# Kernel tuning notes

Measured on AMD Instinct MI355X. Metric: run time of the kernel, lower is better.

## Reference

```python
import jax, jax.numpy as jnp
import numpy as np

D_MODEL, N_HEADS, D_FF = 512, 8, 2048
B, L = 2, 2048


def layer_norm(x, g, b, eps=1e-5):
    mu = jnp.mean(x, axis=-1, keepdims=True)
    var = jnp.mean(jnp.square(x - mu), axis=-1, keepdims=True)
    return (x - mu) * jax.lax.rsqrt(var + eps) * g + b


def setup_inputs() -> dict:
    key = jax.random.key(0)
    ks = jax.random.split(key, 16)
    s = 1.0 / np.sqrt(D_MODEL)
    sf = 1.0 / np.sqrt(D_FF)
    return {
        "x": jax.random.normal(ks[0], (B, L, D_MODEL), jnp.float32),
        "Wq": jax.random.normal(ks[1], (D_MODEL, D_MODEL), jnp.float32) * s,
        "bq": jnp.zeros((D_MODEL,), jnp.float32),
        "Wk": jax.random.normal(ks[2], (D_MODEL, D_MODEL), jnp.float32) * s,
        "bk": jnp.zeros((D_MODEL,), jnp.float32),
        "Wv": jax.random.normal(ks[3], (D_MODEL, D_MODEL), jnp.float32) * s,
        "bv": jnp.zeros((D_MODEL,), jnp.float32),
        "Wo": jax.random.normal(ks[4], (D_MODEL, D_MODEL), jnp.float32) * s,
        "bo": jnp.zeros((D_MODEL,), jnp.float32),
        "W1": jax.random.normal(ks[5], (D_FF, D_MODEL), jnp.float32) * s,   # conv1 k=1 -> linear
        "b1": jnp.zeros((D_FF,), jnp.float32),
        "W2": jax.random.normal(ks[6], (D_MODEL, D_FF), jnp.float32) * sf,  # conv2 k=1 -> linear
        "b2": jnp.zeros((D_MODEL,), jnp.float32),
        "g1": jnp.ones((D_MODEL,), jnp.float32),
        "be1": jnp.zeros((D_MODEL,), jnp.float32),
        "g2": jnp.ones((D_MODEL,), jnp.float32),
        "be2": jnp.zeros((D_MODEL,), jnp.float32),
    }


def reference(x, Wq, bq, Wk, bk, Wv, bv, Wo, bo, W1, b1, W2, b2, g1, be1, g2, be2):
    Bx, Lx, D = x.shape
    H = N_HEADS
    dk = D // H
    # projections -> [B, L, H, dk]
    q = (x @ Wq.T + bq).reshape(Bx, Lx, H, dk)
    k = (x @ Wk.T + bk).reshape(Bx, Lx, H, dk)
    v = (x @ Wv.T + bv).reshape(Bx, Lx, H, dk)
    scale = 1.0 / jnp.sqrt(jnp.asarray(dk, x.dtype))
    scores = jnp.einsum('blhd,bshd->bhls', q, k)  # full LxL score tensor (as in source)
    A = jax.nn.softmax(scale * scores, axis=-1)
    out = jnp.einsum('bhls,bshd->blhd', A, v).reshape(Bx, Lx, D)
    attn_out = out @ Wo.T + bo
    # residual + norm1 (dropout is identity in eval)
    x1 = layer_norm(x + attn_out, g1, be1)
    # FFN: conv1d with kernel_size=1 == pointwise linear
    y = jax.nn.relu(x1 @ W1.T + b1)
    y = y @ W2.T + b2
    return layer_norm(x1 + y, g2, be2)
```

## Files before the change

### kernel.cpp

```cpp
#include <hip/hip_runtime.h>
#include <hip/hip_bf16.h>
#include <cstddef>

#define SEQ 2048
#define DM  512
#define NH  8
#define DKH 64
#define DFF 2048
#define NB  2
#define MR  (NB*SEQ)

typedef __attribute__((ext_vector_type(8))) short short8;
typedef __attribute__((ext_vector_type(4))) float f32x4;

#define AS1(p) ((const __attribute__((address_space(1))) void*)(p))
#define AS3(p) ((__attribute__((address_space(3))) void*)(p))
#define LGKM0() do { asm volatile("s_waitcnt lgkmcnt(0)" ::: "memory"); \
                     __builtin_amdgcn_sched_barrier(0); } while (0)

#define QSCALE 0.180336880f

__device__ inline unsigned cvtpk(float lo, float hi) {
  unsigned r;
  asm("v_cvt_pk_bf16_f32 %0, %1, %2" : "=v"(r) : "v"(lo), "v"(hi));
  return r;
}

__device__ inline void cvt8(const float* __restrict__ s, __hip_bfloat16* __restrict__ d) {
  float4 a = *reinterpret_cast<const float4*>(s);
  float4 b = *reinterpret_cast<const float4*>(s + 4);
  union { __hip_bfloat16 h[8]; short8 v; } u;
  u.h[0] = __float2bfloat16(a.x); u.h[1] = __float2bfloat16(a.y);
  u.h[2] = __float2bfloat16(a.z); u.h[3] = __float2bfloat16(a.w);
  u.h[4] = __float2bfloat16(b.x); u.h[5] = __float2bfloat16(b.y);
  u.h[6] = __float2bfloat16(b.z); u.h[7] = __float2bfloat16(b.w);
  *reinterpret_cast<short8*>(d) = u.v;
}

__global__ __launch_bounds__(256) void cvt_all(
    const float* __restrict__ x,
    const float* __restrict__ Wq, const float* __restrict__ Wk,
    const float* __restrict__ Wv, const float* __restrict__ Wo,
    const float* __restrict__ W1, const float* __restrict__ W2,
    const float* __restrict__ bq, const float* __restrict__ bk,
    const float* __restrict__ bv,
    __hip_bfloat16* __restrict__ xb,  __hip_bfloat16* __restrict__ wqkv,
    __hip_bfloat16* __restrict__ wob, __hip_bfloat16* __restrict__ w1b,
    __hip_bfloat16* __restrict__ w2b, float* __restrict__ bqkv)
{
  const int u = blockIdx.x * 256 + threadIdx.x;
  if (u < 262144) {
    cvt8(x + (size_t)u * 8, xb + (size_t)u * 8);
  } else if (u < 360448) {
    const int d = (u - 262144) * 8;
    const int n = d >> 9, k = d & 511;
    const float* src = (n < 512) ? (Wq + (size_t)n * 512 + k)
                     : (n < 1024) ? (Wk + (size_t)(n - 512) * 512 + k)
                                  : (Wv + (size_t)(n - 1024) * 512 + k);
    cvt8(src, wqkv + d);
  } else if (u < 393216) {
    const int d = (u - 360448) * 8; cvt8(Wo + d, wob + d);
  } else if (u < 524288) {
    const int d = (u - 393216) * 8; cvt8(W1 + d, w1b + d);
  } else if (u < 655360) {
    const int d = (u - 524288) * 8; cvt8(W2 + d, w2b + d);
  } else if (u < 655552) {
    const int d = (u - 655360) * 8;
    const float* src = (d < 512) ? (bq + d) : (d < 1024) ? (bk + d - 512) : (bv + d - 1024);
    *reinterpret_cast<float4*>(bqkv + d)     = *reinterpret_cast<const float4*>(src);
    *reinterpret_cast<float4*>(bqkv + d + 4) = *reinterpret_cast<const float4*>(src + 4);
  }
}

template<int OUT_BF16, int RELU, int WVT, int SPLITK>
__global__ __launch_bounds__(256) void gemm_bt(
    const __hip_bfloat16* __restrict__ A, const __hip_bfloat16* __restrict__ Bt,
    const float* __restrict__ bias, void* __restrict__ Cout, void* __restrict__ Cout1,
    __hip_bfloat16* __restrict__ qkbO, __hip_bfloat16* __restrict__ vtO,
    int M, int N, int K)
{
  __shared__ __align__(16) char lds[32768];
  char* Asm = lds;
  char* Bsm = lds + 16384;
  const int t = threadIdx.x, lane = t & 63, w = t >> 6;
  const int m0 = blockIdx.y * 128, n0 = blockIdx.x * 128;
  const int wm = w >> 1, wn = w & 1;
  const int z = (SPLITK == 2) ? blockIdx.z : 0;
  const int Keff = (SPLITK == 2) ? (K >> 1) : K;
  const int koff = z * Keff;
  const int g = lane >> 4;

  const int r0   = t >> 3;
  const int kofs = ((lane & 7) ^ (r0 & 7)) * 8;
  const __hip_bfloat16* ap = A  + (size_t)(m0 + r0) * K + koff + kofs;
  const __hip_bfloat16* bp = Bt + (size_t)(n0 + r0) * K + koff + kofs;
  const int ldsoff = t * 16;

  const int fA = (wm * 64 + (lane & 15)) * 128;
  const int fB = (wn * 64 + (lane & 15)) * 128;
  const int sw = lane & 7;

  f32x4 acc[4][4] = {};

  const int nkt = Keff >> 6;
  for (int kt = 0; kt < nkt; ++kt) {
    const size_t ko = (size_t)kt * 64;
#pragma unroll
    for (int ii = 0; ii < 4; ++ii) {
      __builtin_amdgcn_global_load_lds(AS1(ap + (size_t)ii * 32 * K + ko), AS3(Asm + ii * 4096 + ldsoff), 16, 0, 0);
      __builtin_amdgcn_global_load_lds(AS1(bp + (size_t)ii * 32 * K + ko), AS3(Bsm + ii * 4096 + ldsoff), 16, 0, 0);
    }
    __syncthreads();
#pragma unroll
    for (int kk = 0; kk < 2; ++kk) {
      const int cx = ((kk * 4 + g) ^ sw) * 16;
      short8 af[4], bf[4];
#pragma unroll
      for (int i = 0; i < 4; ++i) af[i] = *reinterpret_cast<const short8*>(Asm + fA + i * 2048 + cx);
#pragma unroll
      for (int j = 0; j < 4; ++j) bf[j] = *reinterpret_cast<const short8*>(Bsm + fB + j * 2048 + cx);
      __builtin_amdgcn_s_setprio(1);
#pragma unroll
      for (int i = 0; i < 4; ++i)
#pragma unroll
        for (int j = 0; j < 4; ++j)
          acc[i][j] = __builtin_amdgcn_mfma_f32_16x16x32_bf16(af[i], bf[j], acc[i][j], 0, 0, 0);
      __builtin_amdgcn_s_setprio(0);
    }
    __syncthreads();
  }

  float bcol[4];
#pragma unroll
  for (int j = 0; j < 4; ++j)
    bcol[j] = (SPLITK == 2 && z) ? 0.f : bias[n0 + wn * 64 + j * 16 + (lane & 15)];

  if (WVT && n0 >= 1024) {
#pragma unroll
    for (int i = 0; i < 4; ++i) {
      const int r = m0 + wm * 64 + i * 16 + (g << 2);
      const int bb = r >> 11, s = r & 2047;
#pragma unroll
      for (int j = 0; j < 4; ++j) {
        const int hd = n0 + wn * 64 + j * 16 + (lane & 15) - 1024;
        union { __hip_bfloat16 h[4]; uint2 uu; } pk;
#pragma unroll
        for (int jj = 0; jj < 4; ++jj) pk.h[jj] = __float2bfloat16(acc[i][j][jj] + bcol[j]);
        *reinterpret_cast<uint2*>(vtO + ((size_t)(bb * 8 + (hd >> 6)) * 64 + (hd & 63)) * SEQ + s) = pk.uu;
      }
    }
    return;
  }

  const float qsc = (WVT && n0 < 512) ? QSCALE : 1.0f;
#pragma unroll
  for (int i = 0; i < 4; ++i) {
    const int row = m0 + wm * 64 + i * 16 + (g << 2);
#pragma unroll
    for (int j = 0; j < 4; ++j) {
      const int col = n0 + wn * 64 + j * 16 + (lane & 15);
#pragma unroll
      for (int jj = 0; jj < 4; ++jj) {
        float v = acc[i][j][jj] + bcol[j];
        if (RELU) v = fmaxf(v, 0.f);
        if (WVT)
          qkbO[(size_t)(row + jj) * 1024 + col] = __float2bfloat16(v * qsc);
        else if (OUT_BF16)
          ((__hip_bfloat16*)Cout)[(size_t)(row + jj) * N + col] = __float2bfloat16(v);
        else {
          float* dst = (float*)((SPLITK == 2 && z) ? Cout1 : Cout);
          dst[(size_t)(row + jj) * N + col] = v;
        }
      }
    }
  }
}

__global__ __launch_bounds__(256) void attn_mfma(
    const __hip_bfloat16* __restrict__ qkb, const __hip_bfloat16* __restrict__ vtb,
    float* __restrict__ po, float* __restrict__ pm, float* __restrict__ pl)
{
  __shared__ __align__(16) char lds[32768];
  char* ks = lds;
  char* vT = lds + 16384;
  char* pb = lds + 24576;

  const int t = threadIdx.x, lane = t & 63, w = t >> 6;
  const int qt = blockIdx.x, bh = blockIdx.y, z = blockIdx.z;
  const int b = bh >> 3, h = bh & 7;
  const int ST0 = z * (SEQ / 2);
  const int q = lane & 15, g = lane >> 4;
  const int NT = SEQ / 2 / 64;

  const __hip_bfloat16* Qg = qkb + (size_t)b * SEQ * 1024 + h * DKH;
  const int qr = qt * 64 + w * 16 + q;
  const short8 aq0 = *reinterpret_cast<const short8*>(Qg + (size_t)qr * 1024 + g * 8);
  const short8 aq1 = *reinterpret_cast<const short8*>(Qg + (size_t)qr * 1024 + 32 + g * 8);

  const int srow = t >> 3;
  const int sofs = ((lane & 7) ^ (srow & 7)) * 8;
  const __hip_bfloat16* kbase = qkb + (size_t)(b * SEQ + ST0 + srow) * 1024 + 512 + h * DKH + sofs;
  const __hip_bfloat16* vbase = vtb + ((size_t)bh * 64 + srow) * SEQ + ST0 + sofs;
  const int ldso = t * 16;
  char* pw = pb + w * 2048;
  char* pwq = pw + q * 128;
  const int psw = (q & 7) << 4;

  f32x4 o[4] = {};
  float m_ = -1e30f, l_ = 0.f;

  auto STAGE_K = [&](int buf, int st) {
    const size_t ko = (size_t)st * 64 * 1024;
    char* kd = ks + buf * 8192 + ldso;
    __builtin_amdgcn_global_load_lds(AS1(kbase + ko),                     AS3(kd),        16, 0, 0);
    __builtin_amdgcn_global_load_lds(AS1(kbase + ko + (size_t)32 * 1024), AS3(kd + 4096), 16, 0, 0);
  };
  auto STAGE_V = [&](int st) {
    const size_t vo = (size_t)st * 64;
    char* vd = vT + ldso;
    __builtin_amdgcn_global_load_lds(AS1(vbase + vo),                    AS3(vd),        16, 0, 0);
    __builtin_amdgcn_global_load_lds(AS1(vbase + vo + (size_t)32 * SEQ), AS3(vd + 4096), 16, 0, 0);
  };

  STAGE_K(0, 0);
  __syncthreads();
  int cur = 0;

  for (int st = 0; st < NT; ++st) {
    STAGE_V(st);
    STAGE_K(cur ^ 1, st + 1 < NT ? st + 1 : st);
    const char* kb_ = ks + cur * 8192;

    f32x4 s[4] = {};
    __builtin_amdgcn_s_setprio(1);
#pragma unroll
    for (int kt = 0; kt < 2; ++kt) {
      const int kb = kt * 64 + g * 16;
#pragma unroll
      for (int n = 0; n < 4; ++n) {
        const int row = n * 16 + q;
        const short8 bk = *reinterpret_cast<const short8*>(kb_ + row * 128 + (kb ^ ((row & 7) << 4)));
        s[n] = __builtin_amdgcn_mfma_f32_16x16x32_bf16(bk, kt ? aq1 : aq0, s[n], 0, 0, 0);
      }
    }
    __builtin_amdgcn_s_setprio(0);

    float mx0 = fmaxf(fmaxf(s[0][0], s[0][1]), fmaxf(s[0][2], s[0][3]));
    float mx1 = fmaxf(fmaxf(s[1][0], s[1][1]), fmaxf(s[1][2], s[1][3]));
    float mx2 = fmaxf(fmaxf(s[2][0], s[2][1]), fmaxf(s[2][2], s[2][3]));
    float mx3 = fmaxf(fmaxf(s[3][0], s[3][1]), fmaxf(s[3][2], s[3][3]));
    float pmax = fmaxf(fmaxf(mx0, mx1), fmaxf(mx2, mx3));
    pmax = fmaxf(pmax, __shfl_xor(pmax, 16));
    pmax = fmaxf(pmax, __shfl_xor(pmax, 32));

    const bool skip = __all(pmax <= m_ + 8.0f);
    float al = 1.0f;
    if (!skip) {
      const float mn = fmaxf(m_, pmax);
      al = exp2f(m_ - mn);
      m_ = mn;
    }

    float p[4][4];
    float ps = 0.f;
#pragma unroll
    for (int n = 0; n < 4; ++n) {
      float e0 = exp2f(s[n][0] - m_), e1 = exp2f(s[n][1] - m_);
      float e2 = exp2f(s[n][2] - m_), e3 = exp2f(s[n][3] - m_);
      p[n][0] = e0; p[n][1] = e1; p[n][2] = e2; p[n][3] = e3;
      ps += (e0 + e1) + (e2 + e3);
    }
    ps += __shfl_xor(ps, 16);
    ps += __shfl_xor(ps, 32);
    l_ = l_ * al + ps;
    if (!skip) {
#pragma unroll
      for (int n = 0; n < 4; ++n)
#pragma unroll
        for (int jj = 0; jj < 4; ++jj) o[n][jj] *= al;
    }

#pragma unroll
    for (int n = 0; n < 4; ++n) {
      uint2 uu;
      uu.x = cvtpk(p[n][0], p[n][1]);
      uu.y = cvtpk(p[n][2], p[n][3]);
      *reinterpret_cast<uint2*>(pwq + ((n * 32 + g * 8) ^ psw)) = uu;
    }
    LGKM0();

    asm volatile("s_waitcnt vmcnt(2)" ::: "memory");
    __builtin_amdgcn_s_barrier();
    __builtin_amdgcn_sched_barrier(0);

    __builtin_amdgcn_s_setprio(1);
#pragma unroll
    for (int kt = 0; kt < 2; ++kt) {
      const int kb = kt * 64 + g * 16;
      const short8 app = *reinterpret_cast<const short8*>(pwq + (kb ^ psw));
#pragma unroll
      for (int n = 0; n < 4; ++n) {
        const int vrow = n * 16 + q;
        const short8 av = *reinterpret_cast<const short8*>(vT + vrow * 128 + (kb ^ ((vrow & 7) << 4)));
        o[n] = __builtin_amdgcn_mfma_f32_16x16x32_bf16(av, app, o[n], 0, 0, 0);
      }
    }
    __builtin_amdgcn_s_setprio(0);
    __syncthreads();
    cur ^= 1;
  }

  float* pz = po + (size_t)z * MR * DM;
  {
    const int row = b * SEQ + qt * 64 + w * 16 + q;
    float* dst = pz + (size_t)row * DM + h * DKH;
#pragma unroll
    for (int n = 0; n < 4; ++n)
      *reinterpret_cast<float4*>(dst + n * 16 + g * 4) = *(const float4*)&o[n];
  }
  if (lane < 16) {
    const size_t idx = ((size_t)z * 16 + bh) * SEQ + qt * 64 + w * 16 + q;
    pm[idx] = m_;
    pl[idx] = l_;
  }
}

__global__ __launch_bounds__(256) void attn_combine(
    const float* __restrict__ po, const float* __restrict__ pm,
    const float* __restrict__ pl, __hip_bfloat16* __restrict__ attnb)
{
  const int row  = blockIdx.x * 4 + (threadIdx.x >> 6);
  const int lane = threadIdx.x & 63;
  const int d0 = lane * 8, h = lane >> 3;
  const int b = row >> 11, qq = row & 2047;
  const size_t idx = ((size_t)b * 8 + h) * SEQ + qq;
  const float m0 = pm[idx], m1 = pm[(size_t)16 * SEQ + idx];
  const float l0 = pl[idx], l1 = pl[(size_t)16 * SEQ + idx];
  const float m  = fmaxf(m0, m1);
  const float a0 = exp2f(m0 - m), a1 = exp2f(m1 - m);
  const float inv = 1.0f / (l0 * a0 + l1 * a1);
  const float* p0 = po + (size_t)row * DM + d0;
  const float* p1 = p0 + (size_t)MR * DM;
  float4 x0 = *reinterpret_cast<const float4*>(p0);
  float4 x1 = *reinterpret_cast<const float4*>(p0 + 4);
  float4 y0 = *reinterpret_cast<const float4*>(p1);
  float4 y1 = *reinterpret_cast<const float4*>(p1 + 4);
  union { __hip_bfloat16 hh[8]; short8 v; } u;
  u.hh[0] = __float2bfloat16((x0.x*a0 + y0.x*a1) * inv);
  u.hh[1] = __float2bfloat16((x0.y*a0 + y0.y*a1) * inv);
  u.hh[2] = __float2bfloat16((x0.z*a0 + y0.z*a1) * inv);
  u.hh[3] = __float2bfloat16((x0.w*a0 + y0.w*a1) * inv);
  u.hh[4] = __float2bfloat16((x1.x*a0 + y1.x*a1) * inv);
  u.hh[5] = __float2bfloat16((x1.y*a0 + y1.y*a1) * inv);
  u.hh[6] = __float2bfloat16((x1.z*a0 + y1.z*a1) * inv);
  u.hh[7] = __float2bfloat16((x1.w*a0 + y1.w*a1) * inv);
  *reinterpret_cast<short8*>(attnb + (size_t)row * DM + d0) = u.v;
}

template<int WB>
__global__ __launch_bounds__(256) void ln_res(
    const float* __restrict__ X, const float* __restrict__ Y0,
    const float* __restrict__ Y1,
    const float* __restrict__ g, const float* __restrict__ be,
    float* __restrict__ out, __hip_bfloat16* __restrict__ outb)
{
  const int row  = blockIdx.x * 4 + (threadIdx.x >> 6);
  const int lane = threadIdx.x & 63;
  const int c0   = lane * 8;
  const float* xr = X  + (size_t)row * DM;
  const float* y0 = Y0 + (size_t)row * DM;
  const float* y1 = Y1 + (size_t)row * DM;

  float v[8];
  float4 a0 = *reinterpret_cast<const float4*>(xr + c0);
  float4 a1 = *reinterpret_cast<const float4*>(xr + c0 + 4);
  float4 b0 = *reinterpret_cast<const float4*>(y0 + c0);
  float4 b1 = *reinterpret_cast<const float4*>(y0 + c0 + 4);
  float4 c0v= *reinterpret_cast<const float4*>(y1 + c0);
  float4 c1v= *reinterpret_cast<const float4*>(y1 + c0 + 4);
  v[0]=a0.x+b0.x+c0v.x; v[1]=a0.y+b0.y+c0v.y; v[2]=a0.z+b0.z+c0v.z; v[3]=a0.w+b0.w+c0v.w;
  v[4]=a1.x+b1.x+c1v.x; v[5]=a1.y+b1.y+c1v.y; v[6]=a1.z+b1.z+c1v.z; v[7]=a1.w+b1.w+c1v.w;

  float s = 0.f;
#pragma unroll
  for (int i = 0; i < 8; ++i) s += v[i];
#pragma unroll
  for (int off = 32; off >= 1; off >>= 1) s += __shfl_xor(s, off);
  const float mu = s * (1.0f/512.0f);

  float ss = 0.f;
#pragma unroll
  for (int i = 0; i < 8; ++i) { const float d = v[i] - mu; ss += d*d; }
#pragma unroll
  for (int off = 32; off >= 1; off >>= 1) ss += __shfl_xor(ss, off);
  const float rs = rsqrtf(ss * (1.0f/512.0f) + 1e-5f);

  float4 g0 = *reinterpret_cast<const float4*>(g  + c0);
  float4 g1 = *reinterpret_cast<const float4*>(g  + c0 + 4);
  float4 e0 = *reinterpret_cast<const float4*>(be + c0);
  float4 e1 = *reinterpret_cast<const float4*>(be + c0 + 4);
  float r[8];
  r[0]=(v[0]-mu)*rs*g0.x+e0.x; r[1]=(v[1]-mu)*rs*g0.y+e0.y;
  r[2]=(v[2]-mu)*rs*g0.z+e0.z; r[3]=(v[3]-mu)*rs*g0.w+e0.w;
  r[4]=(v[4]-mu)*rs*g1.x+e1.x; r[5]=(v[5]-mu)*rs*g1.y+e1.y;
  r[6]=(v[6]-mu)*rs*g1.z+e1.z; r[7]=(v[7]-mu)*rs*g1.w+e1.w;
  float4 o0, o1;
  o0.x=r[0]; o0.y=r[1]; o0.z=r[2]; o0.w=r[3];
  o1.x=r[4]; o1.y=r[5]; o1.z=r[6]; o1.w=r[7];
  *reinterpret_cast<float4*>(out + (size_t)row * DM + c0)     = o0;
  *reinterpret_cast<float4*>(out + (size_t)row * DM + c0 + 4) = o1;
  if (WB) {
    union { __hip_bfloat16 h[8]; short8 vv; } u;
#pragma unroll
    for (int i = 0; i < 8; ++i) u.h[i] = __float2bfloat16(r[i]);
    *reinterpret_cast<short8*>(outb + (size_t)row * DM + c0) = u.vv;
  }
}

extern "C" void kernel_launch(void* const* d_in, const int* in_sizes, int n_in,
                              void* d_out, int out_size, void* d_ws, size_t ws_size,
                              hipStream_t stream)
{
  const float* x   = (const float*)d_in[0];
  const float* Wq  = (const float*)d_in[1];
  const float* bq  = (const float*)d_in[2];
  const float* Wk  = (const float*)d_in[3];
  const float* bk  = (const float*)d_in[4];
  const float* Wv  = (const float*)d_in[5];
  const float* bv  = (const float*)d_in[6];
  const float* Wo  = (const float*)d_in[7];
  const float* bo  = (const float*)d_in[8];
  const float* W1  = (const float*)d_in[9];
  const float* b1  = (const float*)d_in[10];
  const float* W2  = (const float*)d_in[11];
  const float* b2  = (const float*)d_in[12];
  const float* g1  = (const float*)d_in[13];
  const float* be1 = (const float*)d_in[14];
  const float* g2  = (const float*)d_in[15];
  const float* be2 = (const float*)d_in[16];
  float* out = (float*)d_out;

  char* p = (char*)d_ws;
  __hip_bfloat16* xb    = (__hip_bfloat16*)p;  p += 4194304;
  __hip_bfloat16* wqkv  = (__hip_bfloat16*)p;  p += 1572864;
  __hip_bfloat16* wob   = (__hip_bfloat16*)p;  p += 524288;
  __hip_bfloat16* w1b   = (__hip_bfloat16*)p;  p += 2097152;
  __hip_bfloat16* w2b   = (__hip_bfloat16*)p;  p += 2097152;
  float*          bqkv  = (float*)p;           p += 8192;
  __hip_bfloat16* qkb   = (__hip_bfloat16*)p;  p += 8388608;
  __hip_bfloat16* vtb   = (__hip_bfloat16*)p;  p += 4194304;
  float*          po    = (float*)p;           p += 16777216;
  float*          pm    = (float*)p;           p += 262144;
  float*          pl    = (float*)p;           p += 262144;
  float*          oproj = (float*)p;           p += 8388608;
  __hip_bfloat16* x1b   = (__hip_bfloat16*)p;  p += 4194304;

  float*          x1    = (float*)qkb;
  __hip_bfloat16* attnb = (__hip_bfloat16*)vtb;
  __hip_bfloat16* f1b   = (__hip_bfloat16*)po;
  float*          y2a   = (float*)d_ws;
  float*          y2b   = oproj;

  const dim3 blk(256);

  cvt_all<<<dim3(2561), blk, 0, stream>>>(x, Wq, Wk, Wv, Wo, W1, W2, bq, bk, bv,
                                          xb, wqkv, wob, w1b, w2b, bqkv);
  gemm_bt<1,0,1,0><<<dim3(12, 32), blk, 0, stream>>>(xb, wqkv, bqkv, nullptr, nullptr, qkb, vtb, MR, 1536, DM);
  attn_mfma   <<<dim3(SEQ/64, NB*NH, 2), blk, 0, stream>>>(qkb, vtb, po, pm, pl);
  attn_combine<<<dim3(MR/4), blk, 0, stream>>>(po, pm, pl, attnb);
  gemm_bt<0,0,0,2><<<dim3(4, 32, 2), blk, 0, stream>>>(attnb, wob, bo, po, po + (size_t)MR*DM, nullptr, nullptr, MR, DM, DM);
  ln_res<1><<<dim3(MR/4), blk, 0, stream>>>(x, po, po + (size_t)MR*DM, g1, be1, x1, x1b);
  gemm_bt<1,1,0,0><<<dim3(16, 32), blk, 0, stream>>>(x1b, w1b, b1, f1b, nullptr, nullptr, nullptr, MR, DFF, DM);
  gemm_bt<0,0,0,2><<<dim3(4, 32, 2), blk, 0, stream>>>(f1b, w2b, b2, y2a, y2b, nullptr, nullptr, MR, DM, DFF);
  ln_res<0><<<dim3(MR/4), blk, 0, stream>>>(x1, y2a, y2b, g2, be2, out, nullptr);
}
```

Before: 136.5 us.

## Switch attention to 32x32 MFMA with register-resident P and 4-way KV split

```diff
diff --git a/kernel.cpp b/kernel.cpp
--- a/kernel.cpp
+++ b/kernel.cpp
@@ -10,13 +10,12 @@
 #define NB  2
 #define MR  (NB*SEQ)
 
-typedef __attribute__((ext_vector_type(8))) short short8;
-typedef __attribute__((ext_vector_type(4))) float f32x4;
+typedef __attribute__((ext_vector_type(8)))  short short8;
+typedef __attribute__((ext_vector_type(4)))  float f32x4;
+typedef __attribute__((ext_vector_type(16))) float f32x16;
 
 #define AS1(p) ((const __attribute__((address_space(1))) void*)(p))
 #define AS3(p) ((__attribute__((address_space(3))) void*)(p))
-#define LGKM0() do { asm volatile("s_waitcnt lgkmcnt(0)" ::: "memory"); \
-                     __builtin_amdgcn_sched_barrier(0); } while (0)
 
 #define QSCALE 0.180336880f
 
@@ -178,35 +177,35 @@
 
 __global__ __launch_bounds__(256) void attn_mfma(
     const __hip_bfloat16* __restrict__ qkb, const __hip_bfloat16* __restrict__ vtb,
-    float* __restrict__ po, float* __restrict__ pm, float* __restrict__ pl)
-{
-  __shared__ __align__(16) char lds[32768];
+    __hip_bfloat16* __restrict__ po, float* __restrict__ pm, float* __restrict__ pl)
+{
+  __shared__ __align__(16) char lds[24576];
   char* ks = lds;
   char* vT = lds + 16384;
-  char* pb = lds + 24576;
 
   const int t = threadIdx.x, lane = t & 63, w = t >> 6;
   const int qt = blockIdx.x, bh = blockIdx.y, z = blockIdx.z;
   const int b = bh >> 3, h = bh & 7;
-  const int ST0 = z * (SEQ / 2);
-  const int q = lane & 15, g = lane >> 4;
-  const int NT = SEQ / 2 / 64;
+  const int ST0 = z * (SEQ / 4);
+  const int NT = SEQ / 4 / 64;
+  const int l31 = lane & 31, hi = lane >> 5;
+  const int swz = (lane & 7) << 4;
+  const int hi16 = hi * 16;
 
   const __hip_bfloat16* Qg = qkb + (size_t)b * SEQ * 1024 + h * DKH;
-  const int qr = qt * 64 + w * 16 + q;
-  const short8 aq0 = *reinterpret_cast<const short8*>(Qg + (size_t)qr * 1024 + g * 8);
-  const short8 aq1 = *reinterpret_cast<const short8*>(Qg + (size_t)qr * 1024 + 32 + g * 8);
+  const int qrow = qt * 128 + w * 32 + l31;
+  short8 qf[4];
+#pragma unroll
+  for (int kc = 0; kc < 4; ++kc)
+    qf[kc] = *reinterpret_cast<const short8*>(Qg + (size_t)qrow * 1024 + kc * 16 + hi * 8);
 
   const int srow = t >> 3;
   const int sofs = ((lane & 7) ^ (srow & 7)) * 8;
   const __hip_bfloat16* kbase = qkb + (size_t)(b * SEQ + ST0 + srow) * 1024 + 512 + h * DKH + sofs;
   const __hip_bfloat16* vbase = vtb + ((size_t)bh * 64 + srow) * SEQ + ST0 + sofs;
   const int ldso = t * 16;
-  char* pw = pb + w * 2048;
-  char* pwq = pw + q * 128;
-  const int psw = (q & 7) << 4;
-
-  f32x4 o[4] = {};
+
+  f32x16 o0 = {}, o1 = {};
   float m_ = -1e30f, l_ = 0.f;
 
   auto STAGE_K = [&](int buf, int st) {
@@ -231,27 +230,26 @@
     STAGE_K(cur ^ 1, st + 1 < NT ? st + 1 : st);
     const char* kb_ = ks + cur * 8192;
 
-    f32x4 s[4] = {};
+    f32x16 acc0 = {}, acc1 = {};
     __builtin_amdgcn_s_setprio(1);
 #pragma unroll
-    for (int kt = 0; kt < 2; ++kt) {
-      const int kb = kt * 64 + g * 16;
-#pragma unroll
-      for (int n = 0; n < 4; ++n) {
-        const int row = n * 16 + q;
-        const short8 bk = *reinterpret_cast<const short8*>(kb_ + row * 128 + (kb ^ ((row & 7) << 4)));
-        s[n] = __builtin_amdgcn_mfma_f32_16x16x32_bf16(bk, kt ? aq1 : aq0, s[n], 0, 0, 0);
-      }
+    for (int kc = 0; kc < 4; ++kc) {
+      const int kbyte = (kc * 32 + hi16) ^ swz;
+      const short8 ka0 = *reinterpret_cast<const short8*>(kb_ + l31 * 128 + kbyte);
+      const short8 ka1 = *reinterpret_cast<const short8*>(kb_ + (32 + l31) * 128 + kbyte);
+      acc0 = __builtin_amdgcn_mfma_f32_32x32x16_bf16(ka0, qf[kc], acc0, 0, 0, 0);
+      acc1 = __builtin_amdgcn_mfma_f32_32x32x16_bf16(ka1, qf[kc], acc1, 0, 0, 0);
     }
     __builtin_amdgcn_s_setprio(0);
 
-    float mx0 = fmaxf(fmaxf(s[0][0], s[0][1]), fmaxf(s[0][2], s[0][3]));
-    float mx1 = fmaxf(fmaxf(s[1][0], s[1][1]), fmaxf(s[1][2], s[1][3]));
-    float mx2 = fmaxf(fmaxf(s[2][0], s[2][1]), fmaxf(s[2][2], s[2][3]));
-    float mx3 = fmaxf(fmaxf(s[3][0], s[3][1]), fmaxf(s[3][2], s[3][3]));
-    float pmax = fmaxf(fmaxf(mx0, mx1), fmaxf(mx2, mx3));
-    pmax = fmaxf(pmax, __shfl_xor(pmax, 16));
-    pmax = fmaxf(pmax, __shfl_xor(pmax, 32));
+    float tm[16];
+#pragma unroll
+    for (int r = 0; r < 16; ++r) tm[r] = fmaxf(acc0[r], acc1[r]);
+#pragma unroll
+    for (int sft = 8; sft >= 1; sft >>= 1)
+#pragma unroll
+      for (int r = 0; r < sft; ++r) tm[r] = fmaxf(tm[r], tm[r + sft]);
+    float pmax = fmaxf(tm[0], __shfl_xor(tm[0], 32));
 
     const bool skip = __all(pmax <= m_ + 8.0f);
     float al = 1.0f;
@@ -261,33 +259,31 @@
       m_ = mn;
     }
 
-    float p[4][4];
+    short8 pf[4];
     float ps = 0.f;
 #pragma unroll
-    for (int n = 0; n < 4; ++n) {
-      float e0 = exp2f(s[n][0] - m_), e1 = exp2f(s[n][1] - m_);
-      float e2 = exp2f(s[n][2] - m_), e3 = exp2f(s[n][3] - m_);
-      p[n][0] = e0; p[n][1] = e1; p[n][2] = e2; p[n][3] = e3;
-      ps += (e0 + e1) + (e2 + e3);
-    }
-    ps += __shfl_xor(ps, 16);
+    for (int sc = 0; sc < 4; ++sc) {
+      const f32x16& A = (sc < 2) ? acc0 : acc1;
+      const int rb = (sc & 1) * 8;
+      float e0 = exp2f(A[rb+0] - m_), e1 = exp2f(A[rb+1] - m_);
+      float e2 = exp2f(A[rb+2] - m_), e3 = exp2f(A[rb+3] - m_);
+      float e4 = exp2f(A[rb+4] - m_), e5 = exp2f(A[rb+5] - m_);
+      float e6 = exp2f(A[rb+6] - m_), e7 = exp2f(A[rb+7] - m_);
+      ps += ((e0 + e1) + (e2 + e3)) + ((e4 + e5) + (e6 + e7));
+      unsigned w0 = cvtpk(e0, e1), w1 = cvtpk(e2, e3);
+      unsigned w2 = cvtpk(e4, e5), w3 = cvtpk(e6, e7);
+      asm("v_permlane32_swap_b32 %0, %1" : "+v"(w0), "+v"(w2));
+      asm("v_permlane32_swap_b32 %0, %1" : "+v"(w1), "+v"(w3));
+      union { unsigned u[4]; short8 s8; } pu;
+      pu.u[0] = w0; pu.u[1] = w1; pu.u[2] = w2; pu.u[3] = w3;
+      pf[sc] = pu.s8;
+    }
     ps += __shfl_xor(ps, 32);
     l_ = l_ * al + ps;
     if (!skip) {
 #pragma unroll
-      for (int n = 0; n < 4; ++n)
-#pragma unroll
-        for (int jj = 0; jj < 4; ++jj) o[n][jj] *= al;
-    }
-
-#pragma unroll
-    for (int n = 0; n < 4; ++n) {
-      uint2 uu;
-      uu.x = cvtpk(p[n][0], p[n][1]);
-      uu.y = cvtpk(p[n][2], p[n][3]);
-      *reinterpret_cast<uint2*>(pwq + ((n * 32 + g * 8) ^ psw)) = uu;
-    }
-    LGKM0();
+      for (int r = 0; r < 16; ++r) { o0[r] *= al; o1[r] *= al; }
+    }
 
     asm volatile("s_waitcnt vmcnt(2)" ::: "memory");
     __builtin_amdgcn_s_barrier();
@@ -295,38 +291,40 @@
 
     __builtin_amdgcn_s_setprio(1);
 #pragma unroll
-    for (int kt = 0; kt < 2; ++kt) {
-      const int kb = kt * 64 + g * 16;
-      const short8 app = *reinterpret_cast<const short8*>(pwq + (kb ^ psw));
-#pragma unroll
-      for (int n = 0; n < 4; ++n) {
-        const int vrow = n * 16 + q;
-        const short8 av = *reinterpret_cast<const short8*>(vT + vrow * 128 + (kb ^ ((vrow & 7) << 4)));
-        o[n] = __builtin_amdgcn_mfma_f32_16x16x32_bf16(av, app, o[n], 0, 0, 0);
-      }
+    for (int sc = 0; sc < 4; ++sc) {
+      const int sbyte = (sc * 32 + hi16) ^ swz;
+      const short8 va0 = *reinterpret_cast<const short8*>(vT + l31 * 128 + sbyte);
+      const short8 va1 = *reinterpret_cast<const short8*>(vT + (32 + l31) * 128 + sbyte);
+      o0 = __builtin_amdgcn_mfma_f32_32x32x16_bf16(va0, pf[sc], o0, 0, 0, 0);
+      o1 = __builtin_amdgcn_mfma_f32_32x32x16_bf16(va1, pf[sc], o1, 0, 0, 0);
     }
     __builtin_amdgcn_s_setprio(0);
     __syncthreads();
     cur ^= 1;
   }
 
-  float* pz = po + (size_t)z * MR * DM;
   {
-    const int row = b * SEQ + qt * 64 + w * 16 + q;
-    float* dst = pz + (size_t)row * DM + h * DKH;
-#pragma unroll
-    for (int n = 0; n < 4; ++n)
-      *reinterpret_cast<float4*>(dst + n * 16 + g * 4) = *(const float4*)&o[n];
-  }
-  if (lane < 16) {
-    const size_t idx = ((size_t)z * 16 + bh) * SEQ + qt * 64 + w * 16 + q;
+    __hip_bfloat16* pz = po + (size_t)z * MR * DM;
+    const size_t orow = (size_t)b * SEQ + qt * 128 + w * 32 + l31;
+    __hip_bfloat16* dst = pz + orow * DM + h * DKH;
+#pragma unroll
+    for (int r = 0; r < 4; ++r) {
+      uint2 u0, u1;
+      u0.x = cvtpk(o0[4*r+0], o0[4*r+1]); u0.y = cvtpk(o0[4*r+2], o0[4*r+3]);
+      u1.x = cvtpk(o1[4*r+0], o1[4*r+1]); u1.y = cvtpk(o1[4*r+2], o1[4*r+3]);
+      *reinterpret_cast<uint2*>(dst + r * 8 + hi * 4)      = u0;
+      *reinterpret_cast<uint2*>(dst + 32 + r * 8 + hi * 4) = u1;
+    }
+  }
+  if (lane < 32) {
+    const size_t idx = ((size_t)z * 16 + bh) * SEQ + qt * 128 + w * 32 + lane;
     pm[idx] = m_;
     pl[idx] = l_;
   }
 }
 
 __global__ __launch_bounds__(256) void attn_combine(
-    const float* __restrict__ po, const float* __restrict__ pm,
+    const __hip_bfloat16* __restrict__ po, const float* __restrict__ pm,
     const float* __restrict__ pl, __hip_bfloat16* __restrict__ attnb)
 {
   const int row  = blockIdx.x * 4 + (threadIdx.x >> 6);
@@ -334,27 +332,29 @@
   const int d0 = lane * 8, h = lane >> 3;
   const int b = row >> 11, qq = row & 2047;
   const size_t idx = ((size_t)b * 8 + h) * SEQ + qq;
-  const float m0 = pm[idx], m1 = pm[(size_t)16 * SEQ + idx];
-  const float l0 = pl[idx], l1 = pl[(size_t)16 * SEQ + idx];
-  const float m  = fmaxf(m0, m1);
-  const float a0 = exp2f(m0 - m), a1 = exp2f(m1 - m);
-  const float inv = 1.0f / (l0 * a0 + l1 * a1);
-  const float* p0 = po + (size_t)row * DM + d0;
-  const float* p1 = p0 + (size_t)MR * DM;
-  float4 x0 = *reinterpret_cast<const float4*>(p0);
-  float4 x1 = *reinterpret_cast<const float4*>(p0 + 4);
-  float4 y0 = *reinterpret_cast<const float4*>(p1);
-  float4 y1 = *reinterpret_cast<const float4*>(p1 + 4);
-  union { __hip_bfloat16 hh[8]; short8 v; } u;
-  u.hh[0] = __float2bfloat16((x0.x*a0 + y0.x*a1) * inv);
-  u.hh[1] = __float2bfloat16((x0.y*a0 + y0.y*a1) * inv);
-  u.hh[2] = __float2bfloat16((x0.z*a0 + y0.z*a1) * inv);
-  u.hh[3] = __float2bfloat16((x0.w*a0 + y0.w*a1) * inv);
-  u.hh[4] = __float2bfloat16((x1.x*a0 + y1.x*a1) * inv);
-  u.hh[5] = __float2bfloat16((x1.y*a0 + y1.y*a1) * inv);
-  u.hh[6] = __float2bfloat16((x1.z*a0 + y1.z*a1) * inv);
-  u.hh[7] = __float2bfloat16((x1.w*a0 + y1.w*a1) * inv);
-  *reinterpret_cast<short8*>(attnb + (size_t)row * DM + d0) = u.v;
+  const size_t zs = (size_t)16 * SEQ;
+  const float m0 = pm[idx], m1 = pm[idx + zs], m2 = pm[idx + 2*zs], m3 = pm[idx + 3*zs];
+  const float l0 = pl[idx], l1 = pl[idx + zs], l2 = pl[idx + 2*zs], l3 = pl[idx + 3*zs];
+  const float M = fmaxf(fmaxf(m0, m1), fmaxf(m2, m3));
+  const float a0 = exp2f(m0 - M), a1 = exp2f(m1 - M);
+  const float a2 = exp2f(m2 - M), a3 = exp2f(m3 - M);
+  const float inv = 1.0f / (l0*a0 + l1*a1 + l2*a2 + l3*a3);
+  float az[4] = {a0, a1, a2, a3};
+  float acc[8] = {};
+  const size_t ro = (size_t)row * DM + d0;
+#pragma unroll
+  for (int zz = 0; zz < 4; ++zz) {
+    short8 v = *reinterpret_cast<const short8*>(po + (size_t)zz * MR * DM + ro);
+#pragma unroll
+    for (int j = 0; j < 8; ++j) {
+      const unsigned uu = ((unsigned)(unsigned short)v[j]) << 16;
+      acc[j] += az[zz] * __builtin_bit_cast(float, uu);
+    }
+  }
+  union { __hip_bfloat16 hh[8]; short8 s8; } u;
+#pragma unroll
+  for (int j = 0; j < 8; ++j) u.hh[j] = __float2bfloat16(acc[j] * inv);
+  *reinterpret_cast<short8*>(attnb + ro) = u.s8;
 }
 
 template<int WB>
@@ -449,15 +449,16 @@
   float*          bqkv  = (float*)p;           p += 8192;
   __hip_bfloat16* qkb   = (__hip_bfloat16*)p;  p += 8388608;
   __hip_bfloat16* vtb   = (__hip_bfloat16*)p;  p += 4194304;
-  float*          po    = (float*)p;           p += 16777216;
-  float*          pm    = (float*)p;           p += 262144;
-  float*          pl    = (float*)p;           p += 262144;
+  __hip_bfloat16* pob   = (__hip_bfloat16*)p;  p += 16777216;
+  float*          pm    = (float*)p;           p += 524288;
+  float*          pl    = (float*)p;           p += 524288;
   float*          oproj = (float*)p;           p += 8388608;
   __hip_bfloat16* x1b   = (__hip_bfloat16*)p;  p += 4194304;
 
   float*          x1    = (float*)qkb;
   __hip_bfloat16* attnb = (__hip_bfloat16*)vtb;
-  __hip_bfloat16* f1b   = (__hip_bfloat16*)po;
+  float*          opa   = (float*)pob;
+  __hip_bfloat16* f1b   = pob;
   float*          y2a   = (float*)d_ws;
   float*          y2b   = oproj;
 
@@ -466,10 +467,10 @@
   cvt_all<<<dim3(2561), blk, 0, stream>>>(x, Wq, Wk, Wv, Wo, W1, W2, bq, bk, bv,
                                           xb, wqkv, wob, w1b, w2b, bqkv);
   gemm_bt<1,0,1,0><<<dim3(12, 32), blk, 0, stream>>>(xb, wqkv, bqkv, nullptr, nullptr, qkb, vtb, MR, 1536, DM);
-  attn_mfma   <<<dim3(SEQ/64, NB*NH, 2), blk, 0, stream>>>(qkb, vtb, po, pm, pl);
-  attn_combine<<<dim3(MR/4), blk, 0, stream>>>(po, pm, pl, attnb);
-  gemm_bt<0,0,0,2><<<dim3(4, 32, 2), blk, 0, stream>>>(attnb, wob, bo, po, po + (size_t)MR*DM, nullptr, nullptr, MR, DM, DM);
-  ln_res<1><<<dim3(MR/4), blk, 0, stream>>>(x, po, po + (size_t)MR*DM, g1, be1, x1, x1b);
+  attn_mfma   <<<dim3(SEQ/128, NB*NH, 4), blk, 0, stream>>>(qkb, vtb, pob, pm, pl);
+  attn_combine<<<dim3(MR/4), blk, 0, stream>>>(pob, pm, pl, attnb);
+  gemm_bt<0,0,0,2><<<dim3(4, 32, 2), blk, 0, stream>>>(attnb, wob, bo, opa, oproj, nullptr, nullptr, MR, DM, DM);
+  ln_res<1><<<dim3(MR/4), blk, 0, stream>>>(x, opa, oproj, g1, be1, x1, x1b);
   gemm_bt<1,1,0,0><<<dim3(16, 32), blk, 0, stream>>>(x1b, w1b, b1, f1b, nullptr, nullptr, nullptr, MR, DFF, DM);
   gemm_bt<0,0,0,2><<<dim3(4, 32, 2), blk, 0, stream>>>(f1b, w2b, b2, y2a, y2b, nullptr, nullptr, MR, DM, DFF);
   ln_res<0><<<dim3(MR/4), blk, 0, stream>>>(x1, y2a, y2b, g2, be2, out, nullptr);
```

Measured after the change: 134.5 us. No clear change (-1.5%).
